# Kernel optimization log

Measured on AMD Instinct MI355X. Metric: run time of the kernel, lower is better.

The kernel has to match this reference:

```python
import jax, jax.numpy as jnp
import numpy as np

EPS = 1e-5

def _ada_ln(x, c, W_ss, b_ss):
    # LayerNorm without affine, then conditional scale/bias from c via SiLU->Linear
    mu = jnp.mean(x, axis=-1, keepdims=True)
    var = jnp.mean((x - mu) ** 2, axis=-1, keepdims=True)
    h = (x - mu) / jnp.sqrt(var + EPS)
    ss = jax.nn.silu(c) @ W_ss + b_ss            # [B, 2H]
    scale, bias = jnp.split(ss, 2, axis=-1)      # [B, H] each
    return (1.0 + scale)[:, None, :] * h + bias[:, None, :]

def setup_inputs() -> dict:
    key = jax.random.key(0)
    ks = jax.random.split(key, 12)
    B, Lq, Lkv, H = 8, 2048, 512, 1024
    s = 0.02
    return {
        "x_q": jax.random.normal(ks[0], (B, Lq, H), jnp.float32),
        "x_kv": jax.random.normal(ks[1], (B, Lkv, H), jnp.float32),
        "t_vec": jax.random.normal(ks[2], (B, H), jnp.float32),
        "Wq": jax.random.normal(ks[3], (H, H), jnp.float32) * s,
        "bq": jnp.zeros((H,), jnp.float32),
        "Wkv": jax.random.normal(ks[4], (H, 2 * H), jnp.float32) * s,
        "bkv": jnp.zeros((2 * H,), jnp.float32),
        "Wp": jax.random.normal(ks[5], (H, H), jnp.float32) * s,
        "bp": jnp.zeros((H,), jnp.float32),
        "Wss_q": jax.random.normal(ks[6], (H, 2 * H), jnp.float32) * s,
        "bss_q": jnp.zeros((2 * H,), jnp.float32),
        "Wss_kv": jax.random.normal(ks[7], (H, 2 * H), jnp.float32) * s,
        "bss_kv": jnp.zeros((2 * H,), jnp.float32),
    }

def reference(x_q, x_kv, t_vec, Wq, bq, Wkv, bkv, Wp, bp, Wss_q, bss_q, Wss_kv, bss_kv):
    B, Lq, H = x_q.shape
    Lkv = x_kv.shape[1]
    nh = 16
    dh = H // nh

    xq = _ada_ln(x_q, t_vec, Wss_q, bss_q)
    xkv = _ada_ln(x_kv, t_vec, Wss_kv, bss_kv)

    q = (xq @ Wq + bq).reshape(B, Lq, nh, dh)          # [B,Lq,h,d]
    kv = (xkv @ Wkv + bkv).reshape(B, Lkv, 2, nh, dh)
    k = kv[:, :, 0]                                     # [B,Lkv,h,d]
    v = kv[:, :, 1]

    scores = jnp.einsum("bqhd,bkhd->bhqk", q, k) / jnp.sqrt(jnp.float32(dh))
    attn = jax.nn.softmax(scores, axis=-1)
    out = jnp.einsum("bhqk,bkhd->bqhd", attn, v).reshape(B, Lq, H)
    return x_q + (out @ Wp + bp)
```

## Files before the change

kernel.cpp:

```cpp
#include <hip/hip_runtime.h>
#include <hip/hip_bf16.h>
#include <stdint.h>

typedef __attribute__((ext_vector_type(8))) short bf16x8;
typedef __attribute__((ext_vector_type(4))) float f32x4;
typedef __attribute__((ext_vector_type(4))) _Float16 f16x4;
typedef __attribute__((ext_vector_type(8))) _Float16 f16x8;
typedef __attribute__((ext_vector_type(4))) unsigned short u16x4;

__device__ __forceinline__ float b2f(unsigned short u){
  union { unsigned int i; float f; } x; x.i = ((unsigned int)u) << 16; return x.f;
}
__device__ __forceinline__ unsigned short f2b(float f){
  union { float f; unsigned int i; } x; x.f = f;
  unsigned int r = x.i + 0x7fffu + ((x.i >> 16) & 1u);
  return (unsigned short)(r >> 16);
}

__device__ __forceinline__ void gld_lds16(const void* g, void* l){
  __builtin_amdgcn_global_load_lds((const __attribute__((address_space(1))) unsigned int*)g,
                                   (__attribute__((address_space(3))) unsigned int*)l,
                                   16, 0, 0);
}

__global__ __launch_bounds__(256) void transpose_k(const float* __restrict__ in,
                                                   unsigned short* __restrict__ out,
                                                   int R, int C){
  __shared__ unsigned short tile[32][33];
  int tx = threadIdx.x & 31, ty = threadIdx.x >> 5;
  int r0 = blockIdx.y * 32, c0 = blockIdx.x * 32;
#pragma unroll
  for (int t = 0; t < 4; ++t)
    tile[ty + t*8][tx] = f2b(in[(size_t)(r0 + ty + t*8) * C + c0 + tx]);
  __syncthreads();
#pragma unroll
  for (int t = 0; t < 4; ++t)
    out[(size_t)(c0 + ty + t*8) * R + r0 + tx] = tile[tx][ty + t*8];
}

__global__ __launch_bounds__(256) void ss_init_k(const float* __restrict__ bssq,
                                                 const float* __restrict__ bssk,
                                                 float* __restrict__ ss_q,
                                                 float* __restrict__ ss_kv){
  int idx = blockIdx.x*256 + threadIdx.x;
  int which = idx >> 14, rem = idx & 16383;
  int j = rem & 2047;
  if (which) ss_kv[rem] = bssk[j];
  else       ss_q[rem]  = bssq[j];
}

__global__ __launch_bounds__(256) void ss2_k(const float* __restrict__ tvec,
                                             const float* __restrict__ Wssq,
                                             const float* __restrict__ Wssk,
                                             float* __restrict__ ss_q,
                                             float* __restrict__ ss_kv){
  const int which = blockIdx.z;
  const float* W = which ? Wssk : Wssq;
  float* ss = which ? ss_kv : ss_q;
  const int col = blockIdx.x*256 + threadIdx.x;
  const int k0 = blockIdx.y*64;

  __shared__ float sl[8][64];
  int idx = threadIdx.x;
#pragma unroll
  for (int t = 0; t < 2; ++t){
    int i = idx + t*256;
    int b = i >> 6, k = i & 63;
    float c = tvec[b*1024 + k0 + k];
    sl[b][k] = c / (1.f + __expf(-c));
  }
  __syncthreads();

  float acc[8] = {0.f,0.f,0.f,0.f,0.f,0.f,0.f,0.f};
#pragma unroll 8
  for (int k = 0; k < 64; ++k){
    float w = W[(size_t)(k0 + k)*2048 + col];
#pragma unroll
    for (int b = 0; b < 8; ++b) acc[b] += sl[b][k] * w;
  }
#pragma unroll
  for (int b = 0; b < 8; ++b)
    atomicAdd(&ss[b*2048 + col], acc[b]);
}

__global__ __launch_bounds__(256) void ada_ln_k(const float* __restrict__ x,
                                                const float* __restrict__ ss,
                                                unsigned short* __restrict__ out,
                                                int L){
  int row = blockIdx.x;
  int b = row / L;
  const float* xr = x + (size_t)row * 1024;
  int tid = threadIdx.x;
  float4 v = *(const float4*)&xr[tid*4];
  float s = v.x + v.y + v.z + v.w;
  __shared__ float red[4];
#pragma unroll
  for (int o = 32; o > 0; o >>= 1) s += __shfl_xor(s, o, 64);
  if ((tid & 63) == 0) red[tid >> 6] = s;
  __syncthreads();
  float mu = (red[0]+red[1]+red[2]+red[3]) * (1.f/1024.f);
  __syncthreads();
  float vs = (v.x-mu)*(v.x-mu) + (v.y-mu)*(v.y-mu) + (v.z-mu)*(v.z-mu) + (v.w-mu)*(v.w-mu);
#pragma unroll
  for (int o = 32; o > 0; o >>= 1) vs += __shfl_xor(vs, o, 64);
  if ((tid & 63) == 0) red[tid >> 6] = vs;
  __syncthreads();
  float var = (red[0]+red[1]+red[2]+red[3]) * (1.f/1024.f);
  float inv = rsqrtf(var + 1e-5f);
  const float* sb = ss + (size_t)b*2048;
  float4 sc = *(const float4*)&sb[tid*4];
  float4 bi = *(const float4*)&sb[1024 + tid*4];
  u16x4 o4;
  o4[0] = f2b((1.f + sc.x) * ((v.x-mu)*inv) + bi.x);
  o4[1] = f2b((1.f + sc.y) * ((v.y-mu)*inv) + bi.y);
  o4[2] = f2b((1.f + sc.z) * ((v.z-mu)*inv) + bi.z);
  o4[3] = f2b((1.f + sc.w) * ((v.w-mu)*inv) + bi.w);
  *(u16x4*)&out[(size_t)row*1024 + tid*4] = o4;
}

__global__ __launch_bounds__(256) void gemm_bt_k(const unsigned short* __restrict__ A,
                                                 const unsigned short* __restrict__ BT,
                                                 const float* __restrict__ bias,
                                                 const float* __restrict__ resf,
                                                 unsigned short* __restrict__ Cb,
                                                 float* __restrict__ Cf,
                                                 _Float16* __restrict__ vT,
                                                 int M, int N, int K, int mode){
  __shared__ __attribute__((aligned(16))) unsigned short As[2][128*64];
  __shared__ __attribute__((aligned(16))) unsigned short Bs[2][128*64];
  const int tid = threadIdx.x;
  const int wave = tid >> 6, lane = tid & 63;
  const int lm = lane & 15, quad = lane >> 4;

  const int gx = gridDim.x;
  const int nwg = gx * gridDim.y;
  const int lid = blockIdx.y * gx + blockIdx.x;
  const int chunk = nwg >> 3;
  const int tile = (lid & 7) * chunk + (lid >> 3);
  const int m0 = (tile / gx) * 128, n0 = (tile % gx) * 128;

  const int wm = (wave >> 1) * 64, wn = (wave & 1) * 64;
  f32x4 acc[4][4];
#pragma unroll
  for (int i = 0; i < 4; ++i)
#pragma unroll
    for (int j = 0; j < 4; ++j) acc[i][j] = (f32x4){0.f,0.f,0.f,0.f};

  int rowc[4], colc[4];
#pragma unroll
  for (int r = 0; r < 4; ++r){
    int c = r*256 + tid;
    rowc[r] = c >> 3; colc[r] = (c & 7) * 8;
  }

#define STAGE128(buf, kk)                                                              \
  {                                                                                    \
    _Pragma("unroll")                                                                  \
    for (int r = 0; r < 4; ++r)                                                        \
      gld_lds16(&A[(size_t)(m0 + rowc[r])*K + (kk) + colc[r]], &As[buf][(r*256 + tid)*8]); \
    _Pragma("unroll")                                                                  \
    for (int r = 0; r < 4; ++r)                                                        \
      gld_lds16(&BT[(size_t)(n0 + rowc[r])*K + (kk) + colc[r]], &Bs[buf][(r*256 + tid)*8]); \
  }

  const int NT = K >> 6;
  STAGE128(0, 0);
  STAGE128(1, 64);
  asm volatile("s_waitcnt vmcnt(8)" ::: "memory");
  __builtin_amdgcn_s_barrier();

  for (int t = 0; t < NT; ++t){
    const int cur = t & 1;
#pragma unroll
    for (int ks = 0; ks < 2; ++ks){
      bf16x8 af[4], bfr[4];
#pragma unroll
      for (int i = 0; i < 4; ++i)
        af[i] = *(bf16x8*)&As[cur][(wm + i*16 + lm)*64 + ks*32 + quad*8];
#pragma unroll
      for (int j = 0; j < 4; ++j)
        bfr[j] = *(bf16x8*)&Bs[cur][(wn + j*16 + lm)*64 + ks*32 + quad*8];
#pragma unroll
      for (int i = 0; i < 4; ++i)
#pragma unroll
        for (int j = 0; j < 4; ++j)
          acc[i][j] = __builtin_amdgcn_mfma_f32_16x16x32_bf16(af[i], bfr[j], acc[i][j], 0, 0, 0);
    }
    if (t + 1 < NT){
      __builtin_amdgcn_s_barrier();
      if (t + 2 < NT){
        STAGE128(cur, (t + 2) << 6);
        asm volatile("s_waitcnt vmcnt(8)" ::: "memory");
      } else {
        asm volatile("s_waitcnt vmcnt(0)" ::: "memory");
      }
      __builtin_amdgcn_s_barrier();
    }
  }
#undef STAGE128

  if (mode == 2 && n0 >= 1024){
#pragma unroll
    for (int j = 0; j < 4; ++j){
      int col = n0 + wn + j*16 + lm;
      int d = col - 1024;
      float bv = bias[col];
#pragma unroll
      for (int i = 0; i < 4; ++i){
        int rowb = m0 + wm + i*16 + quad*4;
        int brow = rowb >> 9, l = rowb & 511;
        f16x4 h4;
#pragma unroll
        for (int p = 0; p < 4; ++p) h4[p] = (_Float16)(acc[i][j][p] + bv);
        *(f16x4*)&vT[((size_t)brow*1024 + d)*512 + l] = h4;
      }
    }
    return;
  }

#pragma unroll
  for (int j = 0; j < 4; ++j){
    int col = n0 + wn + j*16 + lm;
    float bv = bias[col];
#pragma unroll
    for (int i = 0; i < 4; ++i){
#pragma unroll
      for (int p = 0; p < 4; ++p){
        int row = m0 + wm + i*16 + quad*4 + p;
        float v = acc[i][j][p] + bv;
        if (mode == 1){
          Cf[(size_t)row*N + col] = v + resf[(size_t)row*N + col];
        } else {
          Cb[(size_t)row*1024 + col] = f2b(v);
        }
      }
    }
  }
}

__global__ __launch_bounds__(512) void gemm256_k(const unsigned short* __restrict__ A,
                                                 const unsigned short* __restrict__ BT,
                                                 const float* __restrict__ bias,
                                                 const float* __restrict__ resf,
                                                 unsigned short* __restrict__ Cb,
                                                 float* __restrict__ Cf,
                                                 int M, int N, int K, int mode){
  __shared__ __attribute__((aligned(16))) unsigned short As[2][256*64];
  __shared__ __attribute__((aligned(16))) unsigned short Bs[2][256*64];
  const int tid = threadIdx.x;
  const int wave = tid >> 6, lane = tid & 63;
  const int lm = lane & 15, quad = lane >> 4;

  const int gx = gridDim.x;
  const int nwg = gx * gridDim.y;
  const int lid = blockIdx.y * gx + blockIdx.x;
  const int chunk = nwg >> 3;
  const int tile = (lid & 7) * chunk + (lid >> 3);
  const int m0 = (tile / gx) * 256, n0 = (tile % gx) * 256;

  const int wm = (wave >> 2) * 128, wn = (wave & 3) * 64;

  f32x4 acc[8][4];
#pragma unroll
  for (int i = 0; i < 8; ++i)
#pragma unroll
    for (int j = 0; j < 4; ++j) acc[i][j] = (f32x4){0.f,0.f,0.f,0.f};

  int rowc[4], colsw[4];
#pragma unroll
  for (int r = 0; r < 4; ++r){
    int c = r*512 + tid;
    rowc[r]  = c >> 3;
    colsw[r] = ((c & 7) ^ (rowc[r] & 7)) * 8;
  }

#define STAGE256(buf, kk)                                                              \
  {                                                                                    \
    _Pragma("unroll")                                                                  \
    for (int r = 0; r < 4; ++r)                                                        \
      gld_lds16(&A[(size_t)(m0 + rowc[r])*K + (kk) + colsw[r]], &As[buf][(r*512 + tid)*8]); \
    _Pragma("unroll")                                                                  \
    for (int r = 0; r < 4; ++r)                                                        \
      gld_lds16(&BT[(size_t)(n0 + rowc[r])*K + (kk) + colsw[r]], &Bs[buf][(r*512 + tid)*8]); \
  }

  const int NT = K >> 6;
  STAGE256(0, 0);
  STAGE256(1, 64);
  asm volatile("s_waitcnt vmcnt(8)" ::: "memory");
  __builtin_amdgcn_s_barrier();

  const int rsw = lm & 7;
  for (int t = 0; t < NT; ++t){
    const int cur = t & 1;
#pragma unroll
    for (int ks = 0; ks < 2; ++ks){
      const int rc = ((ks*4 + quad) ^ rsw) * 8;
      bf16x8 af[8], bfr[4];
#pragma unroll
      for (int i = 0; i < 8; ++i)
        af[i] = *(bf16x8*)&As[cur][(wm + i*16 + lm)*64 + rc];
#pragma unroll
      for (int j = 0; j < 4; ++j)
        bfr[j] = *(bf16x8*)&Bs[cur][(wn + j*16 + lm)*64 + rc];
#pragma unroll
      for (int i = 0; i < 8; ++i)
#pragma unroll
        for (int j = 0; j < 4; ++j)
          acc[i][j] = __builtin_amdgcn_mfma_f32_16x16x32_bf16(af[i], bfr[j], acc[i][j], 0, 0, 0);
    }
    if (t + 1 < NT){
      __builtin_amdgcn_s_barrier();
      if (t + 2 < NT){
        STAGE256(cur, (t + 2) << 6);
        asm volatile("s_waitcnt vmcnt(8)" ::: "memory");
      } else {
        asm volatile("s_waitcnt vmcnt(0)" ::: "memory");
      }
      __builtin_amdgcn_s_barrier();
    }
  }
#undef STAGE256

#pragma unroll
  for (int j = 0; j < 4; ++j){
    int col = n0 + wn + j*16 + lm;
    float bv = bias[col];
#pragma unroll
    for (int i = 0; i < 8; ++i){
#pragma unroll
      for (int p = 0; p < 4; ++p){
        int row = m0 + wm + i*16 + quad*4 + p;
        float v = acc[i][j][p] + bv;
        if (mode == 1){
          Cf[(size_t)row*N + col] = v + resf[(size_t)row*N + col];
        } else {
          Cb[(size_t)row*1024 + col] = f2b(v);
        }
      }
    }
  }
}

__global__ __launch_bounds__(256) void attn_k(const unsigned short* __restrict__ q,
                                              const unsigned short* __restrict__ kbuf,
                                              const _Float16* __restrict__ vT,
                                              unsigned short* __restrict__ out){
  const int lid = (blockIdx.z * gridDim.y + blockIdx.y) * gridDim.x + blockIdx.x;
  const int tile = (lid & 7) * 256 + (lid >> 3);
  const int qb = tile & 15, h = (tile >> 4) & 15, b = tile >> 8;
  const int tid = threadIdx.x;
  const int wave = tid >> 6, lane = tid & 63;
  const int lm = lane & 15, quad = lane >> 4;
  const int q0 = qb * 128;

  __shared__ __attribute__((aligned(16))) unsigned short Ks[64*72];
  __shared__ __attribute__((aligned(16))) _Float16      Vs[64*72];

  bf16x8 qf[2][2];
#pragma unroll
  for (int u = 0; u < 2; ++u){
    const unsigned short* qrow = q + ((size_t)b*2048 + q0 + wave*32 + u*16 + lm)*1024 + h*64;
    qf[u][0] = *(const bf16x8*)&qrow[quad*8];
    qf[u][1] = *(const bf16x8*)&qrow[32 + quad*8];
  }

  const unsigned short* kb = kbuf + ((size_t)b*512)*1024 + h*64;
  const _Float16*       vb = vT + ((size_t)b*1024 + h*64)*512;

  f32x4 oacc[2][4];
#pragma unroll
  for (int u = 0; u < 2; ++u)
#pragma unroll
    for (int nt = 0; nt < 4; ++nt) oacc[u][nt] = (f32x4){0.f,0.f,0.f,0.f};
  float m_run[2] = {-1e30f, -1e30f}, l_run[2] = {0.f, 0.f};

  const int srow = tid >> 3, scol = (tid & 7) * 8;

  for (int kt = 0; kt < 8; ++kt){
    const int l0 = kt * 64;
    __syncthreads();
#pragma unroll
    for (int r = 0; r < 2; ++r){
      int row = r*32 + srow;
      *(bf16x8*)&Ks[row*72 + scol] = *(const bf16x8*)&kb[(size_t)(l0 + row)*1024 + scol];
      *(f16x8*)&Vs[row*72 + scol]  = *(const f16x8*)&vb[(size_t)row*512 + l0 + scol];
    }
    __syncthreads();

    f32x4 sacc[2][4];
#pragma unroll
    for (int u = 0; u < 2; ++u)
#pragma unroll
      for (int s = 0; s < 4; ++s) sacc[u][s] = (f32x4){0.f,0.f,0.f,0.f};
#pragma unroll
    for (int s = 0; s < 4; ++s){
      bf16x8 kf0 = *(bf16x8*)&Ks[(s*16 + lm)*72 + quad*8];
      bf16x8 kf1 = *(bf16x8*)&Ks[(s*16 + lm)*72 + 32 + quad*8];
#pragma unroll
      for (int u = 0; u < 2; ++u){
        sacc[u][s] = __builtin_amdgcn_mfma_f32_16x16x32_bf16(kf0, qf[u][0], sacc[u][s], 0, 0, 0);
        sacc[u][s] = __builtin_amdgcn_mfma_f32_16x16x32_bf16(kf1, qf[u][1], sacc[u][s], 0, 0, 0);
      }
    }

    f16x4 pf[2][4];
#pragma unroll
    for (int u = 0; u < 2; ++u){
      float tm = -1e30f;
#pragma unroll
      for (int s = 0; s < 4; ++s)
#pragma unroll
        for (int p = 0; p < 4; ++p) tm = fmaxf(tm, sacc[u][s][p]);
      tm = fmaxf(tm, __shfl_xor(tm, 16, 64));
      tm = fmaxf(tm, __shfl_xor(tm, 32, 64));
      float m_new = fmaxf(m_run[u], tm * 0.125f);
      float alpha = __expf(m_run[u] - m_new);
      m_run[u] = m_new;
      l_run[u] *= alpha;
      float ap[4];
#pragma unroll
      for (int p = 0; p < 4; ++p) ap[p] = __shfl(alpha, quad*4 + p, 64);
#pragma unroll
      for (int nt = 0; nt < 4; ++nt){
        oacc[u][nt][0] *= ap[0]; oacc[u][nt][1] *= ap[1];
        oacc[u][nt][2] *= ap[2]; oacc[u][nt][3] *= ap[3];
      }
#pragma unroll
      for (int s = 0; s < 4; ++s)
#pragma unroll
        for (int p = 0; p < 4; ++p){
          float e = __expf(sacc[u][s][p] * 0.125f - m_new);
          l_run[u] += e;
          pf[u][s][p] = (_Float16)e;
        }
    }

#pragma unroll
    for (int s = 0; s < 4; ++s){
#pragma unroll
      for (int nt = 0; nt < 4; ++nt){
        f16x4 vf = *(const f16x4*)&Vs[(size_t)(nt*16 + lm)*72 + s*16 + quad*4];
#pragma unroll
        for (int u = 0; u < 2; ++u)
          oacc[u][nt] = __builtin_amdgcn_mfma_f32_16x16x16f16(pf[u][s], vf, oacc[u][nt], 0, 0, 0);
      }
    }
  }

#pragma unroll
  for (int u = 0; u < 2; ++u){
    float lr = l_run[u];
    lr += __shfl_xor(lr, 16, 64);
    lr += __shfl_xor(lr, 32, 64);
    float rinv = 1.f / lr;
    float rp[4];
#pragma unroll
    for (int p = 0; p < 4; ++p) rp[p] = __shfl(rinv, quad*4 + p, 64);
    const size_t obase = ((size_t)b*2048 + q0 + wave*32 + u*16) * 1024 + h*64;
#pragma unroll
    for (int nt = 0; nt < 4; ++nt)
#pragma unroll
      for (int p = 0; p < 4; ++p){
        int row = quad*4 + p;
        out[obase + (size_t)row*1024 + nt*16 + lm] = f2b(oacc[u][nt][p] * rp[p]);
      }
  }
}

extern "C" void kernel_launch(void* const* d_in, const int* in_sizes, int n_in,
                              void* d_out, int out_size, void* d_ws, size_t ws_size,
                              hipStream_t stream){
  const float* x_q  = (const float*)d_in[0];
  const float* x_kv = (const float*)d_in[1];
  const float* tvec = (const float*)d_in[2];
  const float* Wq   = (const float*)d_in[3];
  const float* bq   = (const float*)d_in[4];
  const float* Wkv  = (const float*)d_in[5];
  const float* bkv  = (const float*)d_in[6];
  const float* Wp   = (const float*)d_in[7];
  const float* bp   = (const float*)d_in[8];
  const float* Wssq = (const float*)d_in[9];
  const float* bssq = (const float*)d_in[10];
  const float* Wssk = (const float*)d_in[11];
  const float* bssk = (const float*)d_in[12];

  char* ws = (char*)d_ws;
  float*          ss_q  = (float*)(ws + 0);
  float*          ss_kv = (float*)(ws + 65536);
  unsigned short* xq    = (unsigned short*)(ws + 131072);
  unsigned short* xkv   = (unsigned short*)(ws + 33685504);
  unsigned short* qbuf  = (unsigned short*)(ws + 42074112);
  unsigned short* kbuf  = (unsigned short*)(ws + 75628544);
  _Float16*       vTbuf = (_Float16*)     (ws + 84017152);
  unsigned short* WqT   = (unsigned short*)(ws + 92405760);
  unsigned short* WkvT  = (unsigned short*)(ws + 94502912);
  unsigned short* WpT   = (unsigned short*)(ws + 98697216);

  dim3 blk(256);
  transpose_k<<<dim3(32, 32), blk, 0, stream>>>(Wq,  WqT,  1024, 1024);
  transpose_k<<<dim3(64, 32), blk, 0, stream>>>(Wkv, WkvT, 1024, 2048);
  transpose_k<<<dim3(32, 32), blk, 0, stream>>>(Wp,  WpT,  1024, 1024);

  ss_init_k<<<dim3(128), blk, 0, stream>>>(bssq, bssk, ss_q, ss_kv);
  ss2_k<<<dim3(8, 16, 2), blk, 0, stream>>>(tvec, Wssq, Wssk, ss_q, ss_kv);

  ada_ln_k<<<dim3(16384), blk, 0, stream>>>(x_q,  ss_q,  xq,  2048);
  ada_ln_k<<<dim3(4096),  blk, 0, stream>>>(x_kv, ss_kv, xkv, 512);

  gemm256_k<<<dim3(4, 64), dim3(512), 0, stream>>>(xq, WqT, bq, nullptr, qbuf, nullptr,
                                                   16384, 1024, 1024, 0);
  gemm_bt_k<<<dim3(16, 32), blk, 0, stream>>>(xkv, WkvT, bkv, nullptr, kbuf, nullptr, vTbuf,
                                              4096, 2048, 1024, 2);

  attn_k<<<dim3(16, 16, 8), blk, 0, stream>>>(qbuf, kbuf, vTbuf, xq);

  gemm256_k<<<dim3(4, 64), dim3(512), 0, stream>>>(xq, WpT, bp, x_q, nullptr, (float*)d_out,
                                                   16384, 1024, 1024, 1);
}
```

Before: 417.4 us.

## Split GEMM256 K-tiles into half-stages with fine-grained 8-phase load/MFMA interleave

Restructures the 256x256 GEMM main loop so each 64-wide K tile is stored as two 32-wide halves with a new XOR swizzle. Each iteration runs eight phases, and each phase reads fragments, issues a slice of the next global-to-LDS loads, then runs 16 MFMAs under raised wave priority. The goal is to overlap memory traffic with matrix work more evenly than the old load-everything-then-compute schedule, and to reduce the number of fragment registers live at once. In exchange it adds more barriers and more complex vmcnt bookkeeping, and it assumes the number of K tiles is even.

After: 415.2 us. Within noise of the previous version (-0.5%).

```diff
diff --git a/kernel.cpp b/kernel.cpp
--- a/kernel.cpp
+++ b/kernel.cpp
@@ -245,8 +245,8 @@
                                                  unsigned short* __restrict__ Cb,
                                                  float* __restrict__ Cf,
                                                  int M, int N, int K, int mode){
-  __shared__ __attribute__((aligned(16))) unsigned short As[2][256*64];
-  __shared__ __attribute__((aligned(16))) unsigned short Bs[2][256*64];
+  __shared__ __attribute__((aligned(16))) unsigned short As[2][2][8192];
+  __shared__ __attribute__((aligned(16))) unsigned short Bs[2][2][8192];
   const int tid = threadIdx.x;
   const int wave = tid >> 6, lane = tid & 63;
   const int lm = lane & 15, quad = lane >> 4;
@@ -254,9 +254,9 @@
   const int gx = gridDim.x;
   const int nwg = gx * gridDim.y;
   const int lid = blockIdx.y * gx + blockIdx.x;
-  const int chunk = nwg >> 3;
-  const int tile = (lid & 7) * chunk + (lid >> 3);
-  const int m0 = (tile / gx) * 256, n0 = (tile % gx) * 256;
+  const int chunkw = nwg >> 3;
+  const int tileid = (lid & 7) * chunkw + (lid >> 3);
+  const int m0 = (tileid / gx) * 256, n0 = (tileid % gx) * 256;
 
   const int wm = (wave >> 2) * 128, wn = (wave & 3) * 64;
 
@@ -266,61 +266,80 @@
 #pragma unroll
     for (int j = 0; j < 4; ++j) acc[i][j] = (f32x4){0.f,0.f,0.f,0.f};
 
-  int rowc[4], colsw[4];
-#pragma unroll
-  for (int r = 0; r < 4; ++r){
-    int c = r*512 + tid;
-    rowc[r]  = c >> 3;
-    colsw[r] = ((c & 7) ^ (rowc[r] & 7)) * 8;
-  }
-
-#define STAGE256(buf, kk)                                                              \
-  {                                                                                    \
-    _Pragma("unroll")                                                                  \
-    for (int r = 0; r < 4; ++r)                                                        \
-      gld_lds16(&A[(size_t)(m0 + rowc[r])*K + (kk) + colsw[r]], &As[buf][(r*512 + tid)*8]); \
-    _Pragma("unroll")                                                                  \
-    for (int r = 0; r < 4; ++r)                                                        \
-      gld_lds16(&BT[(size_t)(n0 + rowc[r])*K + (kk) + colsw[r]], &Bs[buf][(r*512 + tid)*8]); \
-  }
+  int srow[2], scol0[2];
+#pragma unroll
+  for (int r = 0; r < 2; ++r){
+    int lc = r*512 + tid;
+    srow[r]  = lc >> 2;
+    scol0[r] = ((lc & 3) ^ ((srow[r] >> 1) & 3)) << 3;
+  }
+
+#define STG_A(bufb, ksb, kt)                                                            \
+  { _Pragma("unroll")                                                                   \
+    for (int r = 0; r < 2; ++r)                                                         \
+      gld_lds16(&A[(size_t)(m0 + srow[r])*K + (kt)*64 + (ksb)*32 + scol0[r]],           \
+                &As[bufb][ksb][(r*512 + tid)*8]); }
+#define STG_B(bufb, ksb, kt)                                                            \
+  { _Pragma("unroll")                                                                   \
+    for (int r = 0; r < 2; ++r)                                                         \
+      gld_lds16(&BT[(size_t)(n0 + srow[r])*K + (kt)*64 + (ksb)*32 + scol0[r]],          \
+                &Bs[bufb][ksb][(r*512 + tid)*8]); }
+
+  const int rc = (quad ^ ((lm >> 1) & 3)) * 8;
+  const int arow = (wm + lm)*32 + rc;
+  const int brow = (wn + lm)*32 + rc;
+
+#define PHASE(bufb, mh, ksb, STAGES, VM)                                                \
+  { bf16x8 af[4], bfr[4];                                                               \
+    _Pragma("unroll")                                                                   \
+    for (int i = 0; i < 4; ++i)                                                         \
+      af[i] = *(const bf16x8*)&As[bufb][ksb][arow + ((mh)*4 + i)*512];                  \
+    _Pragma("unroll")                                                                   \
+    for (int j = 0; j < 4; ++j)                                                         \
+      bfr[j] = *(const bf16x8*)&Bs[bufb][ksb][brow + j*512];                            \
+    STAGES;                                                                             \
+    __builtin_amdgcn_s_barrier();                                                       \
+    __builtin_amdgcn_s_setprio(1);                                                      \
+    _Pragma("unroll")                                                                   \
+    for (int i = 0; i < 4; ++i)                                                         \
+      _Pragma("unroll")                                                                 \
+      for (int j = 0; j < 4; ++j)                                                       \
+        acc[(mh)*4 + i][j] =                                                            \
+          __builtin_amdgcn_mfma_f32_16x16x32_bf16(af[i], bfr[j], acc[(mh)*4 + i][j], 0, 0, 0); \
+    __builtin_amdgcn_s_setprio(0);                                                      \
+    VM;                                                                                 \
+    __builtin_amdgcn_s_barrier(); }
 
   const int NT = K >> 6;
-  STAGE256(0, 0);
-  STAGE256(1, 64);
+  const int NU = NT >> 1;
+
+  STG_A(0, 0, 0); STG_B(0, 0, 0);
+  STG_A(0, 1, 0); STG_B(0, 1, 0);
+  STG_A(1, 0, 1); STG_B(1, 0, 1);
   asm volatile("s_waitcnt vmcnt(8)" ::: "memory");
   __builtin_amdgcn_s_barrier();
 
-  const int rsw = lm & 7;
-  for (int t = 0; t < NT; ++t){
-    const int cur = t & 1;
-#pragma unroll
-    for (int ks = 0; ks < 2; ++ks){
-      const int rc = ((ks*4 + quad) ^ rsw) * 8;
-      bf16x8 af[8], bfr[4];
-#pragma unroll
-      for (int i = 0; i < 8; ++i)
-        af[i] = *(bf16x8*)&As[cur][(wm + i*16 + lm)*64 + rc];
-#pragma unroll
-      for (int j = 0; j < 4; ++j)
-        bfr[j] = *(bf16x8*)&Bs[cur][(wn + j*16 + lm)*64 + rc];
-#pragma unroll
-      for (int i = 0; i < 8; ++i)
-#pragma unroll
-        for (int j = 0; j < 4; ++j)
-          acc[i][j] = __builtin_amdgcn_mfma_f32_16x16x32_bf16(af[i], bfr[j], acc[i][j], 0, 0, 0);
-    }
-    if (t + 1 < NT){
-      __builtin_amdgcn_s_barrier();
-      if (t + 2 < NT){
-        STAGE256(cur, (t + 2) << 6);
-        asm volatile("s_waitcnt vmcnt(8)" ::: "memory");
-      } else {
-        asm volatile("s_waitcnt vmcnt(0)" ::: "memory");
-      }
-      __builtin_amdgcn_s_barrier();
-    }
-  }
-#undef STAGE256
+  for (int u = 0; u < NU; ++u){
+    const int t1 = 2*u + 1, t2 = 2*u + 2, t3 = 2*u + 3;
+    const bool nlast = (u + 1 < NU);
+    PHASE(0, 0, 0, { STG_A(1, 1, t1); }, {});
+    PHASE(0, 1, 0, { STG_B(1, 1, t1); },
+          { asm volatile("s_waitcnt vmcnt(8)" ::: "memory"); });
+    PHASE(0, 0, 1, { if (nlast) STG_A(0, 0, t2); }, {});
+    PHASE(0, 1, 1, { if (nlast) STG_B(0, 0, t2); },
+          { if (nlast) asm volatile("s_waitcnt vmcnt(8)" ::: "memory");
+            else       asm volatile("s_waitcnt vmcnt(4)" ::: "memory"); });
+    PHASE(1, 0, 0, { if (nlast) STG_A(0, 1, t2); }, {});
+    PHASE(1, 1, 0, { if (nlast) STG_B(0, 1, t2); },
+          { if (nlast) asm volatile("s_waitcnt vmcnt(8)" ::: "memory");
+            else       asm volatile("s_waitcnt vmcnt(0)" ::: "memory"); });
+    PHASE(1, 0, 1, { if (nlast) STG_A(1, 0, t3); }, {});
+    PHASE(1, 1, 1, { if (nlast) STG_B(1, 0, t3); },
+          { if (nlast) asm volatile("s_waitcnt vmcnt(8)" ::: "memory"); });
+  }
+#undef PHASE
+#undef STG_A
+#undef STG_B
 
 #pragma unroll
   for (int j = 0; j < 4; ++j){
```
